# Kernel tuning notes

Hardware: AMD Instinct MI355X
Metric: run time of the kernel (lower is better)

The kernel has to match this reference:

```python
import jax, jax.numpy as jnp
import numpy as np

N_EMBD = 1024
N_HEADS = 16
B, T = 4, 2048
EPS = 1e-5


def setup_inputs() -> dict:
    key = jax.random.key(0)
    ks = jax.random.split(key, 8)
    C = N_EMBD
    s = 0.02
    return {
        "x": jax.random.normal(ks[0], (B, T, C), dtype=jnp.float32),
        "ln1_w": jnp.ones((C,), jnp.float32),
        "ln1_b": jnp.zeros((C,), jnp.float32),
        "qkv_w": jax.random.normal(ks[1], (C, 3 * C), jnp.float32) * s,
        "qkv_b": jnp.zeros((3 * C,), jnp.float32),
        "proj_w": jax.random.normal(ks[2], (C, C), jnp.float32) * s,
        "proj_b": jnp.zeros((C,), jnp.float32),
        "ln2_w": jnp.ones((C,), jnp.float32),
        "ln2_b": jnp.zeros((C,), jnp.float32),
        "ff_w1": jax.random.normal(ks[3], (C, 4 * C), jnp.float32) * s,
        "ff_b1": jnp.zeros((4 * C,), jnp.float32),
        "ff_w2": jax.random.normal(ks[4], (4 * C, C), jnp.float32) * s,
        "ff_b2": jnp.zeros((C,), jnp.float32),
    }


def _layernorm(x, w, b):
    mu = jnp.mean(x, axis=-1, keepdims=True)
    var = jnp.mean(jnp.square(x - mu), axis=-1, keepdims=True)
    return (x - mu) * jax.lax.rsqrt(var + EPS) * w + b


def _block(x, ln1_w, ln1_b, qkv_w, qkv_b, proj_w, proj_b,
           ln2_w, ln2_b, ff_w1, ff_b1, ff_w2, ff_b2):
    Bb, Tt, C = x.shape
    hd = C // N_HEADS
    h = _layernorm(x, ln1_w, ln1_b)
    qkv = h @ qkv_w + qkv_b  # [B,T,3C]
    q, k, v = jnp.split(qkv, 3, axis=-1)
    q = q.reshape(Bb, Tt, N_HEADS, hd)
    k = k.reshape(Bb, Tt, N_HEADS, hd)
    v = v.reshape(Bb, Tt, N_HEADS, hd)
    # NOTE: original scales by 1/sqrt(C) (full embed dim), not 1/sqrt(head_dim)
    att = jnp.einsum("bqhd,bkhd->bhqk", q, k) * (1.0 / C ** 0.5)
    causal = jnp.tril(jnp.ones((Tt, Tt), dtype=bool))
    att = jnp.where(causal[None, None], att, -jnp.inf)
    att = jax.nn.softmax(att, axis=-1)
    y = jnp.einsum("bhqk,bkhd->bqhd", att, v).reshape(Bb, Tt, C)
    x = x + y @ proj_w + proj_b
    h2 = _layernorm(x, ln2_w, ln2_b)
    ff = jax.nn.relu(h2 @ ff_w1 + ff_b1) @ ff_w2 + ff_b2
    return x + ff


def reference(x, ln1_w, ln1_b, qkv_w, qkv_b, proj_w, proj_b,
              ln2_w, ln2_b, ff_w1, ff_b1, ff_w2, ff_b2):
    return _block(x, ln1_w, ln1_b, qkv_w, qkv_b, proj_w, proj_b,
                  ln2_w, ln2_b, ff_w1, ff_b1, ff_w2, ff_b2)
```

## Files before the change

### kernel.cpp

```cpp
#include <hip/hip_runtime.h>


typedef __attribute__((ext_vector_type(8))) short shortx8;
typedef __attribute__((ext_vector_type(4))) float floatx4;

__device__ __forceinline__ short f2bf(float f) {
  unsigned u = __builtin_bit_cast(unsigned, f);
  u = (u + 0x7fffu + ((u >> 16) & 1u)) >> 16;
  return (short)u;
}
__device__ __forceinline__ float bf2f(short s) {
  return __builtin_bit_cast(float, (unsigned)((unsigned short)s) << 16);
}

__global__ __launch_bounds__(256)
void transpose_cast(const float* __restrict__ in, short* __restrict__ out,
                    int K, int N) {
  __shared__ float tile[32][33];
  const int n0 = blockIdx.x * 32, k0 = blockIdx.y * 32;
  const int tx = threadIdx.x & 31, ty = threadIdx.x >> 5;
  for (int i = 0; i < 32; i += 8)
    tile[ty + i][tx] = in[(size_t)(k0 + ty + i) * N + n0 + tx];
  __syncthreads();
  for (int i = 0; i < 32; i += 8)
    out[(size_t)(n0 + ty + i) * K + k0 + tx] = f2bf(tile[tx][ty + i]);
}

__global__ __launch_bounds__(256)
void layernorm_kernel(const float* __restrict__ x, const float* __restrict__ w,
                      const float* __restrict__ bta, short* __restrict__ out) {
  const int C = 1024;
  const int row = blockIdx.x;
  const float4 v = ((const float4*)(x + (size_t)row * C))[threadIdx.x];
  float s1 = v.x + v.y + v.z + v.w;
  float s2 = v.x * v.x + v.y * v.y + v.z * v.z + v.w * v.w;
  for (int m = 1; m < 64; m <<= 1) { s1 += __shfl_xor(s1, m); s2 += __shfl_xor(s2, m); }
  __shared__ float r1[4], r2[4];
  const int wid = threadIdx.x >> 6, lane = threadIdx.x & 63;
  if (lane == 0) { r1[wid] = s1; r2[wid] = s2; }
  __syncthreads();
  s1 = r1[0] + r1[1] + r1[2] + r1[3];
  s2 = r2[0] + r2[1] + r2[2] + r2[3];
  const float mean = s1 * (1.0f / C);
  const float var = s2 * (1.0f / C) - mean * mean;
  const float rs = rsqrtf(var + 1e-5f);
  const float4 wv = ((const float4*)w)[threadIdx.x];
  const float4 bv = ((const float4*)bta)[threadIdx.x];
  short4 o;
  o.x = f2bf((v.x - mean) * rs * wv.x + bv.x);
  o.y = f2bf((v.y - mean) * rs * wv.y + bv.y);
  o.z = f2bf((v.z - mean) * rs * wv.z + bv.z);
  o.w = f2bf((v.w - mean) * rs * wv.w + bv.w);
  *(short4*)(out + (size_t)row * C + threadIdx.x * 4) = o;
}

template<int FLAGS, typename OutT>
__global__ __launch_bounds__(256, 4)
void gemm_bt(const short* __restrict__ A, int lda,
             const short* __restrict__ Bt, int ldb,
             const float* __restrict__ bias, const float* __restrict__ resid,
             OutT* __restrict__ C, int M, int N, int K) {
  constexpr bool RELU = (FLAGS & 1) != 0;
  constexpr bool RESID = (FLAGS & 2) != 0;
  __shared__ short As[2][128 * 32];
  __shared__ short Bs[2][128 * 32];
  int bmi, bni;
  {
    const int nb = gridDim.x, mb = gridDim.y;
    const int g = blockIdx.x + nb * blockIdx.y;
    if ((mb & 7) == 0) {
      const int xcd = g & 7, l = g >> 3;
      bmi = xcd * (mb >> 3) + l / nb;
      bni = l % nb;
    } else { bmi = blockIdx.y; bni = blockIdx.x; }
  }
  const int bm0 = bmi * 128, bn0 = bni * 128;
  const int tid = threadIdx.x, wid = tid >> 6, lane = tid & 63;
  const int quad = lane >> 4, l15 = lane & 15;
  const int wm = wid & 1, wn = wid >> 1;
  const int srow = lane >> 2, scol = (lane & 3) * 8;
  floatx4 acc[4][4] = {};
  for (int k0 = 0; k0 < K; k0 += 64) {
    for (int i = 0; i < 2; ++i) {
      const int r0 = (wid * 2 + i) * 16;
      const short* ga = A + (size_t)(bm0 + r0 + srow) * lda + k0 + scol;
      const short* gb = Bt + (size_t)(bn0 + r0 + srow) * ldb + k0 + scol;
      __builtin_amdgcn_global_load_lds(
          (const __attribute__((address_space(1))) void*)ga,
          (__attribute__((address_space(3))) void*)&As[0][r0 * 32], 16, 0, 0);
      __builtin_amdgcn_global_load_lds(
          (const __attribute__((address_space(1))) void*)(ga + 32),
          (__attribute__((address_space(3))) void*)&As[1][r0 * 32], 16, 0, 0);
      __builtin_amdgcn_global_load_lds(
          (const __attribute__((address_space(1))) void*)gb,
          (__attribute__((address_space(3))) void*)&Bs[0][r0 * 32], 16, 0, 0);
      __builtin_amdgcn_global_load_lds(
          (const __attribute__((address_space(1))) void*)(gb + 32),
          (__attribute__((address_space(3))) void*)&Bs[1][r0 * 32], 16, 0, 0);
    }
    asm volatile("s_waitcnt vmcnt(0)" ::: "memory");
    __syncthreads();
    {
      shortx8 af[4], bfr[4];
#pragma unroll
      for (int i = 0; i < 4; ++i)
        af[i] = *(const shortx8*)&As[0][(wm * 64 + i * 16 + l15) * 32 + quad * 8];
#pragma unroll
      for (int j = 0; j < 4; ++j)
        bfr[j] = *(const shortx8*)&Bs[0][(wn * 64 + j * 16 + l15) * 32 + quad * 8];
#pragma unroll
      for (int i = 0; i < 4; ++i)
#pragma unroll
        for (int j = 0; j < 4; ++j)
          acc[i][j] = __builtin_amdgcn_mfma_f32_16x16x32_bf16(af[i], bfr[j], acc[i][j], 0, 0, 0);
    }
    {
      shortx8 af[4], bfr[4];
#pragma unroll
      for (int i = 0; i < 4; ++i)
        af[i] = *(const shortx8*)&As[1][(wm * 64 + i * 16 + l15) * 32 + quad * 8];
#pragma unroll
      for (int j = 0; j < 4; ++j)
        bfr[j] = *(const shortx8*)&Bs[1][(wn * 64 + j * 16 + l15) * 32 + quad * 8];
#pragma unroll
      for (int i = 0; i < 4; ++i)
#pragma unroll
        for (int j = 0; j < 4; ++j)
          acc[i][j] = __builtin_amdgcn_mfma_f32_16x16x32_bf16(af[i], bfr[j], acc[i][j], 0, 0, 0);
    }
    __syncthreads();
  }
#pragma unroll
  for (int i = 0; i < 4; ++i) {
    const int row = bm0 + wm * 64 + i * 16 + quad * 4;
#pragma unroll
    for (int j = 0; j < 4; ++j) {
      const int col = bn0 + wn * 64 + j * 16 + l15;
      const float bb = bias[col];
#pragma unroll
      for (int r = 0; r < 4; ++r) {
        float v = acc[i][j][r] + bb;
        if (RELU) v = fmaxf(v, 0.0f);
        if (RESID) v += resid[(size_t)(row + r) * N + col];
        if constexpr (sizeof(OutT) == 2)
          C[(size_t)(row + r) * N + col] = f2bf(v);
        else
          C[(size_t)(row + r) * N + col] = v;
      }
    }
  }
}

#define ATTN_SLOTS 80
#define ATTN_SLOT_SH 4224

__global__ __launch_bounds__(256)
void attention_chunk(const short* __restrict__ qkv, short* __restrict__ y,
                     float* __restrict__ part) {
  constexpr int T = 2048, C = 1024, HD = 64, S3 = 3072;
  __shared__ short Ks[64 * 72];
  __shared__ short Vt[64 * 72];
  __shared__ short Ps[4][16 * 72];
  const int x = blockIdx.x, h = blockIdx.y, b = blockIdx.z;
  int qb, ch;
  if (x < 8)       { qb = x;                 ch = 0; }
  else if (x < 24) { qb = 8 + ((x - 8) >> 1);  ch = (x - 8) & 1; }
  else if (x < 48) { qb = 16 + (x - 24) / 3;   ch = (x - 24) % 3; }
  else             { qb = 24 + ((x - 48) >> 2); ch = (x - 48) & 3; }
  const int kt0 = ch * 8;
  const int kt1 = min(kt0 + 8, qb + 1);
  const int tid = threadIdx.x, wid = tid >> 6, lane = tid & 63;
  const int quad = lane >> 4, l15 = lane & 15;
  const size_t base = (size_t)b * T * S3;
  const int q0 = qb * 64 + wid * 16;
  const short* Qp = qkv + base + (size_t)(q0 + l15) * S3 + h * HD;
  const shortx8 qf0 = *(const shortx8*)(Qp + quad * 8);
  const shortx8 qf1 = *(const shortx8*)(Qp + 32 + quad * 8);
  floatx4 o[4] = {};
  float lsum[4] = {0.f, 0.f, 0.f, 0.f};
  const float scale2 = 0.03125f * 1.44269504088896f;
  const int skey = tid >> 2, sd = (tid & 3) * 16;
  const int vkp = tid & 31, vdb = tid >> 5;
  const int vkE = (vkp >> 4) * 32 + (vkp & 15);
  const short* Kbase = qkv + base + C + h * HD;
  const short* Vbase = qkv + base + 2 * C + h * HD;
  shortx8 pk0, pk1, pv0, pv1;
  {
    const short* Kp = Kbase + (size_t)(kt0 * 64 + skey) * S3 + sd;
    pk0 = *(const shortx8*)Kp;
    pk1 = *(const shortx8*)(Kp + 8);
    const short* Vp = Vbase + (size_t)(kt0 * 64 + vkE) * S3 + vdb * 8;
    pv0 = *(const shortx8*)Vp;
    pv1 = *(const shortx8*)(Vp + 16 * S3);
  }
  for (int kt = kt0; kt < kt1; ++kt) {
    const int key0 = kt * 64;
    __syncthreads();
    *(shortx8*)&Ks[skey * 72 + sd] = pk0;
    *(shortx8*)&Ks[skey * 72 + sd + 8] = pk1;
#pragma unroll
    for (int j = 0; j < 8; ++j) {
      short2 pr = make_short2(pv0[j], pv1[j]);
      *(short2*)&Vt[(vdb * 8 + j) * 72 + 2 * vkp] = pr;
    }
    __syncthreads();
    if (kt + 1 < kt1) {
      const int kn = key0 + 64;
      const short* Kp = Kbase + (size_t)(kn + skey) * S3 + sd;
      pk0 = *(const shortx8*)Kp;
      pk1 = *(const shortx8*)(Kp + 8);
      const short* Vp = Vbase + (size_t)(kn + vkE) * S3 + vdb * 8;
      pv0 = *(const shortx8*)Vp;
      pv1 = *(const shortx8*)(Vp + 16 * S3);
    }
    floatx4 s[4];
#pragma unroll
    for (int nt = 0; nt < 4; ++nt) {
      const short* kb = &Ks[(nt * 16 + l15) * 72 + quad * 8];
      floatx4 a = {};
      a = __builtin_amdgcn_mfma_f32_16x16x32_bf16(qf0, *(const shortx8*)kb, a, 0, 0, 0);
      a = __builtin_amdgcn_mfma_f32_16x16x32_bf16(qf1, *(const shortx8*)(kb + 32), a, 0, 0, 0);
      s[nt] = a;
    }
    short* pw = &Ps[wid][0];
    if (kt != qb) {
#pragma unroll
      for (int r = 0; r < 4; ++r) {
        const float p0 = __builtin_amdgcn_exp2f(s[0][r] * scale2);
        const float p1 = __builtin_amdgcn_exp2f(s[1][r] * scale2);
        const float p2 = __builtin_amdgcn_exp2f(s[2][r] * scale2);
        const float p3 = __builtin_amdgcn_exp2f(s[3][r] * scale2);
        lsum[r] += (p0 + p1) + (p2 + p3);
        unsigned w0, w1;
        asm("v_cvt_pk_bf16_f32 %0, %1, %2" : "=v"(w0) : "v"(p0), "v"(p1));
        asm("v_cvt_pk_bf16_f32 %0, %1, %2" : "=v"(w1) : "v"(p2), "v"(p3));
        unsigned* prow = (unsigned*)&pw[(quad * 4 + r) * 72];
        prow[l15] = w0;
        prow[16 + l15] = w1;
      }
    } else {
#pragma unroll
      for (int r = 0; r < 4; ++r) {
        const int q = q0 + quad * 4 + r;
        float pr[4];
#pragma unroll
        for (int nt = 0; nt < 4; ++nt) {
          float sv = s[nt][r] * scale2;
          if (key0 + nt * 16 + l15 > q) sv = -INFINITY;
          pr[nt] = __builtin_amdgcn_exp2f(sv);
        }
        lsum[r] += (pr[0] + pr[1]) + (pr[2] + pr[3]);
        unsigned w0, w1;
        asm("v_cvt_pk_bf16_f32 %0, %1, %2" : "=v"(w0) : "v"(pr[0]), "v"(pr[1]));
        asm("v_cvt_pk_bf16_f32 %0, %1, %2" : "=v"(w1) : "v"(pr[2]), "v"(pr[3]));
        unsigned* prow = (unsigned*)&pw[(quad * 4 + r) * 72];
        prow[l15] = w0;
        prow[16 + l15] = w1;
      }
    }
    asm volatile("s_waitcnt lgkmcnt(0)" ::: "memory");
#pragma unroll
    for (int kf = 0; kf < 2; ++kf) {
      const shortx8 pa = *(const shortx8*)&Ps[wid][l15 * 72 + kf * 32 + quad * 8];
#pragma unroll
      for (int dt = 0; dt < 4; ++dt) {
        const shortx8 vb = *(const shortx8*)&Vt[(dt * 16 + l15) * 72 + kf * 32 + quad * 8];
        o[dt] = __builtin_amdgcn_mfma_f32_16x16x32_bf16(pa, vb, o[dt], 0, 0, 0);
      }
    }
  }
  float ls[4];
#pragma unroll
  for (int r = 0; r < 4; ++r) {
    float s = lsum[r];
    for (int off = 1; off < 16; off <<= 1) s += __shfl_xor(s, off);
    ls[r] = s;
  }
  if (x < 8) {
    float inv[4];
#pragma unroll
    for (int r = 0; r < 4; ++r) inv[r] = __builtin_amdgcn_rcpf(ls[r]);
#pragma unroll
    for (int dt = 0; dt < 4; ++dt)
#pragma unroll
      for (int r = 0; r < 4; ++r) {
        const int q = q0 + quad * 4 + r;
        y[((size_t)b * T + q) * C + h * HD + dt * 16 + l15] =
            f2bf(o[dt][r] * inv[r]);
      }
  } else {
    short* pp = (short*)part +
                ((size_t)(b * 16 + h) * ATTN_SLOTS + x) * ATTN_SLOT_SH;
    float* pl = (float*)(pp + 4096);
    const int qw = wid * 16;
#pragma unroll
    for (int dt = 0; dt < 4; ++dt)
#pragma unroll
      for (int r = 0; r < 4; ++r)
        pp[(qw + quad * 4 + r) * 64 + dt * 16 + l15] = f2bf(o[dt][r]);
    if (l15 == 0)
#pragma unroll
      for (int r = 0; r < 4; ++r)
        pl[qw + quad * 4 + r] = ls[r];
  }
}

__global__ __launch_bounds__(256)
void attn_reduce(const float* __restrict__ part, short* __restrict__ y) {
  constexpr int T = 2048, C = 1024;
  const int qb = 8 + blockIdx.x, h = blockIdx.y, b = blockIdx.z;
  const int c = qb / 8 + 1;
  int slot0;
  if (qb < 16)      slot0 = 8 + 2 * (qb - 8);
  else if (qb < 24) slot0 = 24 + 3 * (qb - 16);
  else              slot0 = 48 + 4 * (qb - 24);
  const short* rb = (const short*)part +
                    ((size_t)(b * 16 + h) * ATTN_SLOTS + slot0) * ATTN_SLOT_SH;
  const int t = threadIdx.x;
  const int q = t >> 2, dg = (t & 3) * 16;
  float acc[16] = {};
  float ls = 0.f;
  for (int ci = 0; ci < c; ++ci) {
    const short* pp = rb + (size_t)ci * ATTN_SLOT_SH;
    const shortx8 v0 = *(const shortx8*)(pp + q * 64 + dg);
    const shortx8 v1 = *(const shortx8*)(pp + q * 64 + dg + 8);
#pragma unroll
    for (int i = 0; i < 8; ++i) {
      acc[i] += bf2f(v0[i]);
      acc[8 + i] += bf2f(v1[i]);
    }
    ls += *(const float*)(pp + 4096 + 2 * q);
  }
  const float inv = __builtin_amdgcn_rcpf(ls);
  short o16[16];
#pragma unroll
  for (int i = 0; i < 16; ++i) o16[i] = f2bf(acc[i] * inv);
  short* yp = y + ((size_t)b * T + qb * 64 + q) * C + h * 64 + dg;
  *(shortx8*)yp = *(shortx8*)&o16[0];
  *(shortx8*)(yp + 8) = *(shortx8*)&o16[8];
}

__global__ __launch_bounds__(256)
void attention_kernel(const short* __restrict__ qkv, short* __restrict__ y) {
  constexpr int T = 2048, C = 1024, HD = 64, S3 = 3072;
  __shared__ short Ks[64 * 72];
  __shared__ short Vt[64 * 72];
  __shared__ short Ps[4][16 * 72];
  const int qb = blockIdx.x, h = blockIdx.y, b = blockIdx.z;
  const int tid = threadIdx.x, wid = tid >> 6, lane = tid & 63;
  const int quad = lane >> 4, l15 = lane & 15;
  const size_t base = (size_t)b * T * S3;
  const int q0 = qb * 64 + wid * 16;
  const short* Qp = qkv + base + (size_t)(q0 + l15) * S3 + h * HD;
  const shortx8 qf0 = *(const shortx8*)(Qp + quad * 8);
  const shortx8 qf1 = *(const shortx8*)(Qp + 32 + quad * 8);
  floatx4 o[4] = {};
  float lsum[4] = {0.f, 0.f, 0.f, 0.f};
  const float scale2 = 0.03125f * 1.44269504088896f;
  const int skey = tid >> 2, sd = (tid & 3) * 16;
  const int vkp = tid & 31, vdb = tid >> 5;
  for (int kt = 0; kt <= qb; ++kt) {
    const int key0 = kt * 64;
    __syncthreads();
    {
      const short* Kp = qkv + base + (size_t)(key0 + skey) * S3 + C + h * HD + sd;
      shortx8 ka = *(const shortx8*)Kp;
      shortx8 kb = *(const shortx8*)(Kp + 8);
      *(shortx8*)&Ks[skey * 72 + sd] = ka;
      *(shortx8*)&Ks[skey * 72 + sd + 8] = kb;
      const short* Vp = qkv + base + (size_t)(key0 + 2 * vkp) * S3 + 2 * C + h * HD + vdb * 8;
      shortx8 va = *(const shortx8*)Vp;
      shortx8 vb = *(const shortx8*)(Vp + S3);
#pragma unroll
      for (int j = 0; j < 8; ++j) {
        short2 pr = make_short2(va[j], vb[j]);
        *(short2*)&Vt[(vdb * 8 + j) * 72 + 2 * vkp] = pr;
      }
    }
    __syncthreads();
    floatx4 s[4];
#pragma unroll
    for (int nt = 0; nt < 4; ++nt) {
      const short* kb = &Ks[(nt * 16 + l15) * 72 + quad * 8];
      floatx4 a = {};
      a = __builtin_amdgcn_mfma_f32_16x16x32_bf16(qf0, *(const shortx8*)kb, a, 0, 0, 0);
      a = __builtin_amdgcn_mfma_f32_16x16x32_bf16(qf1, *(const shortx8*)(kb + 32), a, 0, 0, 0);
      s[nt] = a;
    }
    short* pw = &Ps[wid][0];
    const bool diag = (kt == qb);
#pragma unroll
    for (int nt = 0; nt < 4; ++nt)
#pragma unroll
      for (int r = 0; r < 4; ++r) {
        float sv = s[nt][r] * scale2;
        if (diag) {
          const int key = key0 + nt * 16 + l15;
          const int q = q0 + quad * 4 + r;
          if (key > q) sv = -INFINITY;
        }
        const float p = __builtin_amdgcn_exp2f(sv);
        lsum[r] += p;
        pw[(quad * 4 + r) * 72 + nt * 16 + l15] = f2bf(p);
      }
    asm volatile("s_waitcnt lgkmcnt(0)" ::: "memory");
#pragma unroll
    for (int kf = 0; kf < 2; ++kf) {
      const shortx8 pa = *(const shortx8*)&Ps[wid][l15 * 72 + kf * 32 + quad * 8];
#pragma unroll
      for (int dt = 0; dt < 4; ++dt) {
        const shortx8 vb = *(const shortx8*)&Vt[(dt * 16 + l15) * 72 + kf * 32 + quad * 8];
        o[dt] = __builtin_amdgcn_mfma_f32_16x16x32_bf16(pa, vb, o[dt], 0, 0, 0);
      }
    }
  }
  float inv[4];
#pragma unroll
  for (int r = 0; r < 4; ++r) {
    float s = lsum[r];
    for (int off = 1; off < 16; off <<= 1) s += __shfl_xor(s, off);
    inv[r] = __builtin_amdgcn_rcpf(s);
  }
#pragma unroll
  for (int dt = 0; dt < 4; ++dt)
#pragma unroll
    for (int r = 0; r < 4; ++r) {
      const int q = q0 + quad * 4 + r;
      y[((size_t)b * T + q) * C + h * HD + dt * 16 + l15] = f2bf(o[dt][r] * inv[r]);
    }
}

extern "C" void kernel_launch(void* const* d_in, const int* in_sizes, int n_in,
                              void* d_out, int out_size, void* d_ws, size_t ws_size,
                              hipStream_t stream) {
  const float* x      = (const float*)d_in[0];
  const float* ln1_w  = (const float*)d_in[1];
  const float* ln1_b  = (const float*)d_in[2];
  const float* qkv_w  = (const float*)d_in[3];
  const float* qkv_b  = (const float*)d_in[4];
  const float* proj_w = (const float*)d_in[5];
  const float* proj_b = (const float*)d_in[6];
  const float* ln2_w  = (const float*)d_in[7];
  const float* ln2_b  = (const float*)d_in[8];
  const float* ff_w1  = (const float*)d_in[9];
  const float* ff_b1  = (const float*)d_in[10];
  const float* ff_w2  = (const float*)d_in[11];
  const float* ff_b2  = (const float*)d_in[12];
  float* out = (float*)d_out;

  char* p = (char*)d_ws;
  short* wT_qkv  = (short*)p; p += (size_t)3072 * 1024 * 2;
  short* wT_proj = (short*)p; p += (size_t)1024 * 1024 * 2;
  short* wT_ff1  = (short*)p; p += (size_t)4096 * 1024 * 2;
  short* wT_ff2  = (short*)p; p += (size_t)1024 * 4096 * 2;
  short* act16   = (short*)p; p += (size_t)8192 * 1024 * 2;
  short* big     = (short*)p; p += (size_t)8192 * 4096 * 2;
  float* part    = (float*)p;
  const size_t need = (size_t)(p - (char*)d_ws) +
                      (size_t)64 * ATTN_SLOTS * ATTN_SLOT_SH * 2;
  const bool split = (ws_size >= need);

  transpose_cast<<<dim3(96, 32), 256, 0, stream>>>(qkv_w, wT_qkv, 1024, 3072);
  transpose_cast<<<dim3(32, 32), 256, 0, stream>>>(proj_w, wT_proj, 1024, 1024);
  transpose_cast<<<dim3(128, 32), 256, 0, stream>>>(ff_w1, wT_ff1, 1024, 4096);
  transpose_cast<<<dim3(32, 128), 256, 0, stream>>>(ff_w2, wT_ff2, 4096, 1024);

  layernorm_kernel<<<8192, 256, 0, stream>>>(x, ln1_w, ln1_b, act16);
  gemm_bt<0, short><<<dim3(24, 64), 256, 0, stream>>>(
      act16, 1024, wT_qkv, 1024, qkv_b, nullptr, big, 8192, 3072, 1024);
  if (split) {
    attention_chunk<<<dim3(ATTN_SLOTS, 16, 4), 256, 0, stream>>>(big, act16, part);
    attn_reduce<<<dim3(24, 16, 4), 256, 0, stream>>>(part, act16);
  } else {
    attention_kernel<<<dim3(32, 16, 4), 256, 0, stream>>>(big, act16);
  }
  gemm_bt<2, float><<<dim3(8, 64), 256, 0, stream>>>(
      act16, 1024, wT_proj, 1024, proj_b, x, out, 8192, 1024, 1024);
  layernorm_kernel<<<8192, 256, 0, stream>>>(out, ln2_w, ln2_b, act16);
  gemm_bt<1, short><<<dim3(32, 64), 256, 0, stream>>>(
      act16, 1024, wT_ff1, 1024, ff_b1, nullptr, big, 8192, 4096, 1024);
  gemm_bt<2, float><<<dim3(8, 64), 256, 0, stream>>>(
      big, 4096, wT_ff2, 4096, ff_b2, out, out, 8192, 1024, 4096);
}
```

Baseline: 501.7 us.

## Widen attention chunks to 128 query rows with 8 warps sharing K/V tiles

The split attention kernel now uses 512-thread blocks covering 128 query rows (two 64-row query blocks), so each staged K/V tile in shared memory serves twice as many queries. K and V loading is split between the two thread halves, which halves per-thread global load work. Warps skip key tiles beyond their own causal limit. The slot count and partial-result layout are halved and doubled accordingly, and the reduce kernel is reworked for 128-row slots. The risks are fewer blocks (less parallelism), idle warps on the diagonal tiles, and higher shared-memory use per block.

```diff
diff --git a/kernel.cpp b/kernel.cpp
--- a/kernel.cpp
+++ b/kernel.cpp
@@ -151,68 +151,78 @@
   }
 }
 
-#define ATTN_SLOTS 80
-#define ATTN_SLOT_SH 4224
-
-__global__ __launch_bounds__(256)
+#define ATTN_SLOTS 40
+#define ATTN_SLOT_SH 8448
+
+__global__ __launch_bounds__(512)
 void attention_chunk(const short* __restrict__ qkv, short* __restrict__ y,
                      float* __restrict__ part) {
   constexpr int T = 2048, C = 1024, HD = 64, S3 = 3072;
   __shared__ short Ks[64 * 72];
   __shared__ short Vt[64 * 72];
-  __shared__ short Ps[4][16 * 72];
+  __shared__ short Ps[8][16 * 72];
   const int x = blockIdx.x, h = blockIdx.y, b = blockIdx.z;
-  int qb, ch;
-  if (x < 8)       { qb = x;                 ch = 0; }
-  else if (x < 24) { qb = 8 + ((x - 8) >> 1);  ch = (x - 8) & 1; }
-  else if (x < 48) { qb = 16 + (x - 24) / 3;   ch = (x - 24) % 3; }
-  else             { qb = 24 + ((x - 48) >> 2); ch = (x - 48) & 3; }
+  int qb0, ch;
+  if (x < 4)       { qb0 = x;                    ch = 0; }
+  else if (x < 12) { qb0 = 4 + ((x - 4) >> 1);   ch = (x - 4) & 1; }
+  else if (x < 24) { qb0 = 8 + (x - 12) / 3;     ch = (x - 12) % 3; }
+  else             { qb0 = 12 + ((x - 24) >> 2); ch = (x - 24) & 3; }
   const int kt0 = ch * 8;
-  const int kt1 = min(kt0 + 8, qb + 1);
+  const int kt1 = min(kt0 + 8, 2 * qb0 + 2);
   const int tid = threadIdx.x, wid = tid >> 6, lane = tid & 63;
   const int quad = lane >> 4, l15 = lane & 15;
+  const int qbw = 2 * qb0 + (wid >> 2);
   const size_t base = (size_t)b * T * S3;
-  const int q0 = qb * 64 + wid * 16;
+  const int q0 = qb0 * 128 + wid * 16;
   const short* Qp = qkv + base + (size_t)(q0 + l15) * S3 + h * HD;
   const shortx8 qf0 = *(const shortx8*)(Qp + quad * 8);
   const shortx8 qf1 = *(const shortx8*)(Qp + 32 + quad * 8);
   floatx4 o[4] = {};
   float lsum[4] = {0.f, 0.f, 0.f, 0.f};
   const float scale2 = 0.03125f * 1.44269504088896f;
-  const int skey = tid >> 2, sd = (tid & 3) * 16;
-  const int vkp = tid & 31, vdb = tid >> 5;
+  const int t2 = tid & 255;
+  const int skey = t2 >> 2, sd = (t2 & 3) * 16;
+  const int vkp = tid & 31, vdb = (tid >> 5) & 7;
   const int vkE = (vkp >> 4) * 32 + (vkp & 15);
   const short* Kbase = qkv + base + C + h * HD;
   const short* Vbase = qkv + base + 2 * C + h * HD;
   shortx8 pk0, pk1, pv0, pv1;
-  {
+  if (tid < 256) {
+    const short* Vp = Vbase + (size_t)(kt0 * 64 + vkE) * S3 + vdb * 8;
+    pv0 = *(const shortx8*)Vp;
+    pv1 = *(const shortx8*)(Vp + 16 * S3);
+  } else {
     const short* Kp = Kbase + (size_t)(kt0 * 64 + skey) * S3 + sd;
     pk0 = *(const shortx8*)Kp;
     pk1 = *(const shortx8*)(Kp + 8);
-    const short* Vp = Vbase + (size_t)(kt0 * 64 + vkE) * S3 + vdb * 8;
-    pv0 = *(const shortx8*)Vp;
-    pv1 = *(const shortx8*)(Vp + 16 * S3);
   }
   for (int kt = kt0; kt < kt1; ++kt) {
     const int key0 = kt * 64;
     __syncthreads();
-    *(shortx8*)&Ks[skey * 72 + sd] = pk0;
-    *(shortx8*)&Ks[skey * 72 + sd + 8] = pk1;
-#pragma unroll
-    for (int j = 0; j < 8; ++j) {
-      short2 pr = make_short2(pv0[j], pv1[j]);
-      *(short2*)&Vt[(vdb * 8 + j) * 72 + 2 * vkp] = pr;
+    if (tid < 256) {
+#pragma unroll
+      for (int j = 0; j < 8; ++j) {
+        short2 pr = make_short2(pv0[j], pv1[j]);
+        *(short2*)&Vt[(vdb * 8 + j) * 72 + 2 * vkp] = pr;
+      }
+    } else {
+      *(shortx8*)&Ks[skey * 72 + sd] = pk0;
+      *(shortx8*)&Ks[skey * 72 + sd + 8] = pk1;
     }
     __syncthreads();
     if (kt + 1 < kt1) {
       const int kn = key0 + 64;
-      const short* Kp = Kbase + (size_t)(kn + skey) * S3 + sd;
-      pk0 = *(const shortx8*)Kp;
-      pk1 = *(const shortx8*)(Kp + 8);
-      const short* Vp = Vbase + (size_t)(kn + vkE) * S3 + vdb * 8;
-      pv0 = *(const shortx8*)Vp;
-      pv1 = *(const shortx8*)(Vp + 16 * S3);
-    }
+      if (tid < 256) {
+        const short* Vp = Vbase + (size_t)(kn + vkE) * S3 + vdb * 8;
+        pv0 = *(const shortx8*)Vp;
+        pv1 = *(const shortx8*)(Vp + 16 * S3);
+      } else {
+        const short* Kp = Kbase + (size_t)(kn + skey) * S3 + sd;
+        pk0 = *(const shortx8*)Kp;
+        pk1 = *(const shortx8*)(Kp + 8);
+      }
+    }
+    if (kt > qbw) continue;
     floatx4 s[4];
 #pragma unroll
     for (int nt = 0; nt < 4; ++nt) {
@@ -223,7 +233,7 @@
       s[nt] = a;
     }
     short* pw = &Ps[wid][0];
-    if (kt != qb) {
+    if (kt != qbw) {
 #pragma unroll
       for (int r = 0; r < 4; ++r) {
         const float p0 = __builtin_amdgcn_exp2f(s[0][r] * scale2);
@@ -276,7 +286,7 @@
     for (int off = 1; off < 16; off <<= 1) s += __shfl_xor(s, off);
     ls[r] = s;
   }
-  if (x < 8) {
+  if (x < 4) {
     float inv[4];
 #pragma unroll
     for (int r = 0; r < 4; ++r) inv[r] = __builtin_amdgcn_rcpf(ls[r]);
@@ -291,53 +301,53 @@
   } else {
     short* pp = (short*)part +
                 ((size_t)(b * 16 + h) * ATTN_SLOTS + x) * ATTN_SLOT_SH;
-    float* pl = (float*)(pp + 4096);
-    const int qw = wid * 16;
+    float* pl = (float*)(pp + 8192);
+    const int rw = wid * 16;
 #pragma unroll
     for (int dt = 0; dt < 4; ++dt)
 #pragma unroll
       for (int r = 0; r < 4; ++r)
-        pp[(qw + quad * 4 + r) * 64 + dt * 16 + l15] = f2bf(o[dt][r]);
+        pp[(rw + quad * 4 + r) * 64 + dt * 16 + l15] = f2bf(o[dt][r]);
     if (l15 == 0)
 #pragma unroll
       for (int r = 0; r < 4; ++r)
-        pl[qw + quad * 4 + r] = ls[r];
+        pl[rw + quad * 4 + r] = ls[r];
   }
 }
 
 __global__ __launch_bounds__(256)
 void attn_reduce(const float* __restrict__ part, short* __restrict__ y) {
   constexpr int T = 2048, C = 1024;
-  const int qb = 8 + blockIdx.x, h = blockIdx.y, b = blockIdx.z;
-  const int c = qb / 8 + 1;
+  const int qb0 = 4 + blockIdx.x, h = blockIdx.y, b = blockIdx.z;
+  const int c = qb0 / 4 + 1;
   int slot0;
-  if (qb < 16)      slot0 = 8 + 2 * (qb - 8);
-  else if (qb < 24) slot0 = 24 + 3 * (qb - 16);
-  else              slot0 = 48 + 4 * (qb - 24);
+  if (qb0 < 8)       slot0 = 4 + 2 * (qb0 - 4);
+  else if (qb0 < 12) slot0 = 12 + 3 * (qb0 - 8);
+  else               slot0 = 24 + 4 * (qb0 - 12);
   const short* rb = (const short*)part +
                     ((size_t)(b * 16 + h) * ATTN_SLOTS + slot0) * ATTN_SLOT_SH;
   const int t = threadIdx.x;
-  const int q = t >> 2, dg = (t & 3) * 16;
-  float acc[16] = {};
+  const int q = t >> 1, dg = (t & 1) * 32;
+  float acc[32] = {};
   float ls = 0.f;
   for (int ci = 0; ci < c; ++ci) {
     const short* pp = rb + (size_t)ci * ATTN_SLOT_SH;
-    const shortx8 v0 = *(const shortx8*)(pp + q * 64 + dg);
-    const shortx8 v1 = *(const shortx8*)(pp + q * 64 + dg + 8);
-#pragma unroll
-    for (int i = 0; i < 8; ++i) {
-      acc[i] += bf2f(v0[i]);
-      acc[8 + i] += bf2f(v1[i]);
-    }
-    ls += *(const float*)(pp + 4096 + 2 * q);
+#pragma unroll
+    for (int v = 0; v < 4; ++v) {
+      const shortx8 w = *(const shortx8*)(pp + q * 64 + dg + 8 * v);
+#pragma unroll
+      for (int i = 0; i < 8; ++i) acc[8 * v + i] += bf2f(w[i]);
+    }
+    ls += ((const float*)(pp + 8192))[q];
   }
   const float inv = __builtin_amdgcn_rcpf(ls);
-  short o16[16];
-#pragma unroll
-  for (int i = 0; i < 16; ++i) o16[i] = f2bf(acc[i] * inv);
-  short* yp = y + ((size_t)b * T + qb * 64 + q) * C + h * 64 + dg;
-  *(shortx8*)yp = *(shortx8*)&o16[0];
-  *(shortx8*)(yp + 8) = *(shortx8*)&o16[8];
+  short o16[32];
+#pragma unroll
+  for (int i = 0; i < 32; ++i) o16[i] = f2bf(acc[i] * inv);
+  short* yp = y + ((size_t)b * T + qb0 * 128 + q) * C + h * 64 + dg;
+#pragma unroll
+  for (int v = 0; v < 4; ++v)
+    *(shortx8*)(yp + 8 * v) = *(shortx8*)&o16[8 * v];
 }
 
 __global__ __launch_bounds__(256)
@@ -469,8 +479,8 @@
   gemm_bt<0, short><<<dim3(24, 64), 256, 0, stream>>>(
       act16, 1024, wT_qkv, 1024, qkv_b, nullptr, big, 8192, 3072, 1024);
   if (split) {
-    attention_chunk<<<dim3(ATTN_SLOTS, 16, 4), 256, 0, stream>>>(big, act16, part);
-    attn_reduce<<<dim3(24, 16, 4), 256, 0, stream>>>(part, act16);
+    attention_chunk<<<dim3(ATTN_SLOTS, 16, 4), 512, 0, stream>>>(big, act16, part);
+    attn_reduce<<<dim3(12, 16, 4), 256, 0, stream>>>(part, act16);
   } else {
     attention_kernel<<<dim3(32, 16, 4), 256, 0, stream>>>(big, act16);
   }
```

Result: no change. 511.5 us (+2.0%).
